# Kernel tuning notes

Hardware: AMD Instinct MI355X
Metric: run time of the kernel (lower is better)

Reference implementation:

```python
import jax, jax.numpy as jnp
import numpy as np

DIM = 512   # feature channels (dim)
K = 3       # depthwise kernel size
H = 256     # grid extent along pos[:,0]
W = 256     # grid extent along pos[:,1]
N = 20000   # number of occupied spots (unique coordinates)


def setup_inputs() -> dict:
    key = jax.random.key(0)
    k1, k2, k3 = jax.random.split(key, 3)
    rng = np.random.default_rng(0)
    # N unique flat cells; pin corners so the dense grid extent is exactly HxW
    flat = np.concatenate([[0, H * W - 1], rng.permutation(H * W - 2)[: N - 2] + 1])
    pos = jnp.asarray(np.stack([flat // W, flat % W], axis=1), dtype=jnp.int32)  # (N,2)
    x = jax.random.normal(k1, (1, N, DIM), jnp.float32)
    weight = jax.random.normal(k2, (DIM, 1, K, K), jnp.float32) * 0.05  # depthwise OIHW
    bias = jax.random.normal(k3, (DIM,), jnp.float32) * 0.05
    return {"x": x, "pos": pos, "weight": weight, "bias": bias}


def reference(x, pos, weight, bias):
    pos = pos - pos.min(axis=0)                 # shift to origin (as torch)
    p0, p1 = pos[:, 0], pos[:, 1]
    xsq = x[0]                                  # (N, DIM)
    # scatter sparse coords to dense grid (duplicates would sum, coords unique)
    grid = jnp.zeros((H, W, DIM), x.dtype).at[p0, p1].add(xsq)   # (H, W, DIM)
    xd = grid.transpose(2, 1, 0)[None]          # (1, DIM, W, H) == permute(2,1,0).unsqueeze(0)
    conv = jax.lax.conv_general_dilated(
        xd, weight, (1, 1), "SAME",
        dimension_numbers=("NCHW", "OIHW", "NCHW"),
        feature_group_count=DIM,
    ) + bias[None, :, None, None]
    mask = xd.sum(axis=1, keepdims=True) != 0.0  # occupied cells
    out_d = jnp.where(mask, conv, 0.0) + xd      # masked residual
    dense = out_d[0].transpose(2, 1, 0)          # (H, W, DIM)
    # gather back to sparse values; torch to_sparse(2) orders rows lexicographically
    order = jnp.lexsort((p1, p0))
    vals = dense[p0[order], p1[order]]           # (N, DIM)
    return vals[None]                            # (1, N, DIM)
```

## Files before the change

kernel.cpp:

```cpp
#include <hip/hip_runtime.h>

#define HH 256
#define WW 256
#define DIM 512

typedef float f32x4 __attribute__((ext_vector_type(4)));


__global__ __launch_bounds__(256) void scatter_kernel(const int* __restrict__ pos,
                                                      int* __restrict__ cell_map,
                                                      int n) {
    int i = blockIdx.x * 256 + threadIdx.x;
    if (i >= n) return;
    int p0 = pos[2 * i];
    int p1 = pos[2 * i + 1];
    cell_map[p0 * WW + p1] = i;
}

__global__ __launch_bounds__(256) void rank_kernel(const int* __restrict__ cell_map,
                                                   int* __restrict__ nbr) {
    __shared__ int red[256];
    __shared__ int wt[4];
    const int t = threadIdx.x;
    const int b = blockIdx.x;
    const int limit = b * 256;

    int cnt = 0;
    const int4* cm4 = (const int4*)cell_map;
    for (int i = t; i * 4 < limit; i += 256) {
        int4 v = cm4[i];
        cnt += (v.x >= 0) + (v.y >= 0) + (v.z >= 0) + (v.w >= 0);
    }
    red[t] = cnt;
    __syncthreads();
    #pragma unroll
    for (int d = 128; d > 0; d >>= 1) {
        if (t < d) red[t] += red[t + d];
        __syncthreads();
    }
    int blk_off = red[0];

    int cell = limit + t;
    int m = cell_map[cell];
    bool occ = (m >= 0);
    unsigned long long mask = __ballot(occ);
    int lane = t & 63;
    int wave = t >> 6;
    int pre = __popcll(mask & ((1ull << lane) - 1ull));
    if (lane == 0) wt[wave] = __popcll(mask);
    __syncthreads();
    int woff = 0;
    for (int i = 0; i < wave; ++i) woff += wt[i];

    if (occ) {
        int rk = blk_off + woff + pre;
        int h = cell >> 8;
        int w = cell & (WW - 1);
        int* row = nbr + rk * 16;
        row[0] = m;
        #pragma unroll
        for (int k = 0; k < 9; ++k) {
            if (k == 4) continue;
            int dh = k % 3 - 1;
            int dw = k / 3 - 1;
            int hh = h + dh;
            int ww = w + dw;
            int v = -1;
            if ((unsigned)hh < (unsigned)HH && (unsigned)ww < (unsigned)WW)
                v = cell_map[hh * WW + ww];
            row[(k < 4 ? k : k - 1) + 1] = v;
        }
    }
}

__global__ __launch_bounds__(256) void conv_main(const float* __restrict__ x,
                                                 const float* __restrict__ weight,
                                                 const float* __restrict__ bias,
                                                 const int* __restrict__ nbr,
                                                 float* __restrict__ out,
                                                 int n) {
    const int lane = threadIdx.x & 63;
    const int wv   = __builtin_amdgcn_readfirstlane(threadIdx.x >> 6);
    const int c0   = lane * 8;

    float wtv[72];
    {
        const float4* wb = (const float4*)(weight + c0 * 9);
        #pragma unroll
        for (int q = 0; q < 18; ++q) {
            float4 v = wb[q];
            wtv[4 * q + 0] = v.x; wtv[4 * q + 1] = v.y;
            wtv[4 * q + 2] = v.z; wtv[4 * q + 3] = v.w;
        }
    }
    float bj[8];
    {
        float4 b0 = *(const float4*)(bias + c0);
        float4 b1 = *(const float4*)(bias + c0 + 4);
        bj[0]=b0.x; bj[1]=b0.y; bj[2]=b0.z; bj[3]=b0.w;
        bj[4]=b1.x; bj[5]=b1.y; bj[6]=b1.z; bj[7]=b1.w;
    }
    #pragma unroll
    for (int j = 0; j < 8; ++j) wtv[j * 9 + 4] += 1.0f;

    const int nbk = gridDim.x;
    const int cid = (blockIdx.x & 7) * (nbk >> 3) + (blockIdx.x >> 3);
    const int ppb = (n + nbk - 1) / nbk;
    const int base = cid * ppb;
    int endr = base + ppb; if (endr > n) endr = n;

    int r = base + wv;
    if (r >= endr) return;

    const int4* nb4 = (const int4*)nbr;
    int4 A = nb4[r * 4 + 0];
    int4 B = nb4[r * 4 + 1];
    int4 C = nb4[r * 4 + 2];

    while (r < endr) {
        const int rn = r + 4;
        int4 An = A, Bn = B, Cn = C;
        if (rn < endr) {
            An = nb4[rn * 4 + 0];
            Bn = nb4[rn * 4 + 1];
            Cn = nb4[rn * 4 + 2];
        }

        const int ms = A.x;
        int m[8];
        m[0]=A.y; m[1]=A.z; m[2]=A.w; m[3]=B.x;
        m[4]=B.y; m[5]=B.z; m[6]=B.w; m[7]=C.x;

        const float* xs = x + (size_t)ms * DIM + c0;
        float4 s0 = *(const float4*)(xs);
        float4 s1 = *(const float4*)(xs + 4);
        float acc[8];
        acc[0] = bj[0] + s0.x * wtv[0*9+4]; acc[1] = bj[1] + s0.y * wtv[1*9+4];
        acc[2] = bj[2] + s0.z * wtv[2*9+4]; acc[3] = bj[3] + s0.w * wtv[3*9+4];
        acc[4] = bj[4] + s1.x * wtv[4*9+4]; acc[5] = bj[5] + s1.y * wtv[5*9+4];
        acc[6] = bj[6] + s1.z * wtv[6*9+4]; acc[7] = bj[7] + s1.w * wtv[7*9+4];

        #pragma unroll
        for (int j = 0; j < 8; ++j) {
            const int k = (j < 4) ? j : j + 1;
            if (m[j] >= 0) {
                const float* xn = x + (size_t)m[j] * DIM + c0;
                float4 n0 = *(const float4*)(xn);
                float4 n1 = *(const float4*)(xn + 4);
                acc[0] += n0.x * wtv[0*9+k]; acc[1] += n0.y * wtv[1*9+k];
                acc[2] += n0.z * wtv[2*9+k]; acc[3] += n0.w * wtv[3*9+k];
                acc[4] += n1.x * wtv[4*9+k]; acc[5] += n1.y * wtv[5*9+k];
                acc[6] += n1.z * wtv[6*9+k]; acc[7] += n1.w * wtv[7*9+k];
            }
        }

        float* op = out + (size_t)r * DIM + c0;
        f32x4 o0 = { acc[0], acc[1], acc[2], acc[3] };
        f32x4 o1 = { acc[4], acc[5], acc[6], acc[7] };
        __builtin_nontemporal_store(o0, (f32x4*)op);
        __builtin_nontemporal_store(o1, (f32x4*)(op + 4));

        r = rn;
        A = An; B = Bn; C = Cn;
    }
}

extern "C" void kernel_launch(void* const* d_in, const int* in_sizes, int n_in,
                              void* d_out, int out_size, void* d_ws, size_t ws_size,
                              hipStream_t stream) {
    const float* x      = (const float*)d_in[0];
    const int*   pos    = (const int*)d_in[1];
    const float* weight = (const float*)d_in[2];
    const float* bias   = (const float*)d_in[3];
    float* out = (float*)d_out;

    int n = in_sizes[1] / 2;

    int* ws       = (int*)d_ws;
    int* cell_map = ws;
    int* nbr      = ws + HH * WW;

    scatter_kernel<<<(n + 255) / 256, 256, 0, stream>>>(pos, cell_map, n);
    rank_kernel<<<256, 256, 0, stream>>>(cell_map, nbr);

    const int nblocks = 768;
    conv_main<<<nblocks, 256, 0, stream>>>(x, weight, bias, nbr, out, n);
}
```

Baseline: 121.9 us.

## Split rows into channel halves and double-buffer neighbor gathers across rows

Each wave now handles half of a row's channels (4 per lane instead of 8), which doubles the number of work items and halves the weight registers. The main loop is software-pipelined with two register buffers: it issues all nine neighbor loads for the next item before computing the current one, so gather latency overlaps with FMA work. This is meant to raise memory-level parallelism and occupancy in a latency-bound gather. The cost is that neighbor indices are read twice (once per half) and more float4 registers are live for the two buffers.

```diff
diff --git a/kernel.cpp b/kernel.cpp
--- a/kernel.cpp
+++ b/kernel.cpp
@@ -73,6 +73,42 @@
     }
 }
 
+#define META(tt, A, B, C) { int rr_ = (tt) >> 1;            \
+    A = nb4[rr_ * 4 + 0]; B = nb4[rr_ * 4 + 1]; C = nb4[rr_ * 4 + 2]; }
+
+#define ISSUE(A, B, C, L, mk) {                             \
+    int ms_ = A.x;                                          \
+    L[8] = *(const float4*)(xc + (size_t)ms_ * DIM);        \
+    int mm_[8] = {A.y, A.z, A.w, B.x, B.y, B.z, B.w, C.x};  \
+    mk = 0;                                                 \
+    _Pragma("unroll")                                       \
+    for (int j_ = 0; j_ < 8; ++j_) {                        \
+        if (mm_[j_] >= 0) {                                 \
+            L[j_] = *(const float4*)(xc + (size_t)mm_[j_] * DIM); \
+            mk |= 1 << j_;                                  \
+        }                                                   \
+    } }
+
+#define COMPUTE(mk, L, tt) {                                \
+    float4 s_ = L[8];                                       \
+    float a0 = bj[0] + s_.x * wtv[0*9+4];                   \
+    float a1 = bj[1] + s_.y * wtv[1*9+4];                   \
+    float a2 = bj[2] + s_.z * wtv[2*9+4];                   \
+    float a3 = bj[3] + s_.w * wtv[3*9+4];                   \
+    _Pragma("unroll")                                       \
+    for (int j_ = 0; j_ < 8; ++j_) {                        \
+        const int k_ = (j_ < 4) ? j_ : j_ + 1;              \
+        if (mk & (1 << j_)) {                               \
+            a0 += L[j_].x * wtv[0*9+k_];                    \
+            a1 += L[j_].y * wtv[1*9+k_];                    \
+            a2 += L[j_].z * wtv[2*9+k_];                    \
+            a3 += L[j_].w * wtv[3*9+k_];                    \
+        }                                                   \
+    }                                                       \
+    float* op_ = out + (size_t)((tt) >> 1) * DIM + c0;      \
+    f32x4 o_ = { a0, a1, a2, a3 };                          \
+    __builtin_nontemporal_store(o_, (f32x4*)op_); }
+
 __global__ __launch_bounds__(256) void conv_main(const float* __restrict__ x,
                                                  const float* __restrict__ weight,
                                                  const float* __restrict__ bias,
@@ -81,87 +117,66 @@
                                                  int n) {
     const int lane = threadIdx.x & 63;
     const int wv   = __builtin_amdgcn_readfirstlane(threadIdx.x >> 6);
-    const int c0   = lane * 8;
-
-    float wtv[72];
+
+    const int nbk = gridDim.x;
+    const int cid = (blockIdx.x & 7) * (nbk >> 3) + (blockIdx.x >> 3);
+    const int T   = 2 * n;
+    const int ppb = (T + nbk - 1) / nbk;
+    const int base = cid * ppb;
+    int endt = base + ppb; if (endt > T) endt = T;
+
+    int t = base + wv;
+    if (t >= endt) return;
+
+    const int hf = t & 1;
+    const int c0 = hf * (DIM / 2) + lane * 4;
+
+    float wtv[36];
     {
         const float4* wb = (const float4*)(weight + c0 * 9);
         #pragma unroll
-        for (int q = 0; q < 18; ++q) {
+        for (int q = 0; q < 9; ++q) {
             float4 v = wb[q];
             wtv[4 * q + 0] = v.x; wtv[4 * q + 1] = v.y;
             wtv[4 * q + 2] = v.z; wtv[4 * q + 3] = v.w;
         }
     }
-    float bj[8];
+    float bj[4];
     {
         float4 b0 = *(const float4*)(bias + c0);
-        float4 b1 = *(const float4*)(bias + c0 + 4);
         bj[0]=b0.x; bj[1]=b0.y; bj[2]=b0.z; bj[3]=b0.w;
-        bj[4]=b1.x; bj[5]=b1.y; bj[6]=b1.z; bj[7]=b1.w;
     }
     #pragma unroll
-    for (int j = 0; j < 8; ++j) wtv[j * 9 + 4] += 1.0f;
-
-    const int nbk = gridDim.x;
-    const int cid = (blockIdx.x & 7) * (nbk >> 3) + (blockIdx.x >> 3);
-    const int ppb = (n + nbk - 1) / nbk;
-    const int base = cid * ppb;
-    int endr = base + ppb; if (endr > n) endr = n;
-
-    int r = base + wv;
-    if (r >= endr) return;
-
+    for (int j = 0; j < 4; ++j) wtv[j * 9 + 4] += 1.0f;
+
+    const float* xc = x + c0;
     const int4* nb4 = (const int4*)nbr;
-    int4 A = nb4[r * 4 + 0];
-    int4 B = nb4[r * 4 + 1];
-    int4 C = nb4[r * 4 + 2];
-
-    while (r < endr) {
-        const int rn = r + 4;
-        int4 An = A, Bn = B, Cn = C;
-        if (rn < endr) {
-            An = nb4[rn * 4 + 0];
-            Bn = nb4[rn * 4 + 1];
-            Cn = nb4[rn * 4 + 2];
-        }
-
-        const int ms = A.x;
-        int m[8];
-        m[0]=A.y; m[1]=A.z; m[2]=A.w; m[3]=B.x;
-        m[4]=B.y; m[5]=B.z; m[6]=B.w; m[7]=C.x;
-
-        const float* xs = x + (size_t)ms * DIM + c0;
-        float4 s0 = *(const float4*)(xs);
-        float4 s1 = *(const float4*)(xs + 4);
-        float acc[8];
-        acc[0] = bj[0] + s0.x * wtv[0*9+4]; acc[1] = bj[1] + s0.y * wtv[1*9+4];
-        acc[2] = bj[2] + s0.z * wtv[2*9+4]; acc[3] = bj[3] + s0.w * wtv[3*9+4];
-        acc[4] = bj[4] + s1.x * wtv[4*9+4]; acc[5] = bj[5] + s1.y * wtv[5*9+4];
-        acc[6] = bj[6] + s1.z * wtv[6*9+4]; acc[7] = bj[7] + s1.w * wtv[7*9+4];
-
-        #pragma unroll
-        for (int j = 0; j < 8; ++j) {
-            const int k = (j < 4) ? j : j + 1;
-            if (m[j] >= 0) {
-                const float* xn = x + (size_t)m[j] * DIM + c0;
-                float4 n0 = *(const float4*)(xn);
-                float4 n1 = *(const float4*)(xn + 4);
-                acc[0] += n0.x * wtv[0*9+k]; acc[1] += n0.y * wtv[1*9+k];
-                acc[2] += n0.z * wtv[2*9+k]; acc[3] += n0.w * wtv[3*9+k];
-                acc[4] += n1.x * wtv[4*9+k]; acc[5] += n1.y * wtv[5*9+k];
-                acc[6] += n1.z * wtv[6*9+k]; acc[7] += n1.w * wtv[7*9+k];
-            }
-        }
-
-        float* op = out + (size_t)r * DIM + c0;
-        f32x4 o0 = { acc[0], acc[1], acc[2], acc[3] };
-        f32x4 o1 = { acc[4], acc[5], acc[6], acc[7] };
-        __builtin_nontemporal_store(o0, (f32x4*)op);
-        __builtin_nontemporal_store(o1, (f32x4*)(op + 4));
-
-        r = rn;
-        A = An; B = Bn; C = Cn;
+
+    int4 Aa, Ba, Ca, Ab, Bb, Cb;
+    float4 La[9], Lb[9];
+    int ma, mb;
+
+    int ta = t;
+    META(ta, Aa, Ba, Ca);
+    int tb = ta + 4;
+    bool hb = (tb < endt);
+    if (hb) META(tb, Ab, Bb, Cb);
+    ISSUE(Aa, Ba, Ca, La, ma);
+
+    for (;;) {
+        if (!hb) { COMPUTE(ma, La, ta); break; }
+        ISSUE(Ab, Bb, Cb, Lb, mb);
+        int tna = tb + 4;
+        bool ha = (tna < endt);
+        if (ha) META(tna, Aa, Ba, Ca);
+        COMPUTE(ma, La, ta);
+        if (!ha) { COMPUTE(mb, Lb, tb); break; }
+        ISSUE(Aa, Ba, Ca, La, ma);
+        int tnb = tna + 4;
+        hb = (tnb < endt);
+        if (hb) META(tnb, Ab, Bb, Cb);
+        COMPUTE(mb, Lb, tb);
+        ta = tna; tb = tnb;
     }
 }
 
```

Measured after the change: 118.2 us, median of 2. -3.0%, faster.
